# Kernel tuning notes

Hardware: AMD Instinct MI355X
Metric: run time of the kernel (lower is better)

## Reference

```python
import jax, jax.numpy as jnp
import numpy as np
from jax import lax

T, B, D = 1024, 32, 1024


def setup_inputs() -> dict:
    key = jax.random.key(0)
    k1, k2, k3, k4 = jax.random.split(key, 4)
    xav = (6.0 / (D + D)) ** 0.5  # xavier_uniform bound
    return {
        "x": jax.random.normal(k1, (T, B, D), dtype=jnp.float32),
        "h0": jnp.zeros((B, D), dtype=jnp.float32),
        "W_alpha": jax.random.uniform(k2, (D, D), minval=-xav, maxval=xav, dtype=jnp.float32),
        "d_alpha": jnp.full((D,), 0.1, dtype=jnp.float32),
        "b_alpha": jnp.full((D,), 2.0, dtype=jnp.float32),
        "W_x": jax.random.uniform(k3, (D, D), minval=-xav, maxval=xav, dtype=jnp.float32),
        "b_v": jnp.zeros((D,), dtype=jnp.float32),
    }


def reference(x, h0, W_alpha, d_alpha, b_alpha, W_x, b_v):
    # Precompute batched GEMMs once (x_t @ W.T), as in the original.
    alpha_x = jnp.einsum("tbd,ed->tbe", x, W_alpha)          # [T,B,D]
    v = jnp.tanh(jnp.einsum("tbd,ed->tbe", x, W_x) + b_v)    # [T,B,D]

    def step(h_prev, inp):
        ax_t, v_t = inp
        alpha = jax.nn.sigmoid(ax_t + d_alpha * h_prev + b_alpha)
        h_new = alpha * h_prev + (1.0 - alpha) * v_t
        out = h_new * h_new * jax.nn.sigmoid(h_new)  # h * silu(h)
        return h_new, (h_new, out)

    _, (hs, outs) = lax.scan(step, h0, (alpha_x, v))
    h = jnp.concatenate([h0[None], hs], axis=0)  # [T+1,B,D]
    return outs, h
```

## Files before the change

kernel.cpp:

```cpp
#include <hip/hip_runtime.h>
#include <hip/hip_bf16.h>
#include <stdint.h>

#define TT 1024
#define BB 32
#define DD 1024
#define MROWS (TT*BB)
#define NCOLS (2*DD)
#define KDIM  (DD)
#define SS (BB*DD)

typedef __attribute__((ext_vector_type(8))) short short8;
typedef __attribute__((ext_vector_type(4))) float f32x4;

__device__ __forceinline__ float bf2f(uint16_t u){
  union { uint32_t u; float f; } c; c.u = ((uint32_t)u) << 16; return c.f;
}
__device__ __forceinline__ uint16_t f2bf(float f){
  union { float f; uint32_t u; } c; c.f = f;
  uint32_t u = c.u;
  u += 0x7FFFu + ((u >> 16) & 1u);
  return (uint16_t)(u >> 16);
}
__device__ __forceinline__ float tanh_fast(float x){
  return 1.f - 2.f/(1.f + __expf(2.f*x));
}
__device__ __forceinline__ float sigmoid_fast(float x){
  return __builtin_amdgcn_rcpf(1.f + __expf(-x));
}

__global__ __launch_bounds__(256) void cvt_x_kernel(const float* __restrict__ x,
                                                    uint16_t* __restrict__ xb, int n4){
  int i = blockIdx.x * 256 + threadIdx.x;
  int stride = gridDim.x * 256;
  for (; i < n4; i += stride){
    float4 f = ((const float4*)x)[i];
    ushort4 o;
    o.x = f2bf(f.x); o.y = f2bf(f.y); o.z = f2bf(f.z); o.w = f2bf(f.w);
    ((ushort4*)xb)[i] = o;
  }
}

__global__ __launch_bounds__(256) void cvt_w_kernel(const float* __restrict__ Wa,
                                                    const float* __restrict__ Wx,
                                                    uint16_t* __restrict__ wc){
  int i = blockIdx.x * 256 + threadIdx.x;
  const int c    = i >> 8;
  const int col4 = i & 255;
  const int e = ((c >> 5) << 4) | (c & 15);
  const int s = (c >> 4) & 1;
  const float* src = (s ? Wx : Wa) + (size_t)e*DD + col4*4;
  float4 f = *(const float4*)src;
  ushort4 o;
  o.x = f2bf(f.x); o.y = f2bf(f.y); o.z = f2bf(f.z); o.w = f2bf(f.w);
  ((ushort4*)wc)[i] = o;
}

__global__ __launch_bounds__(512, 2) void gemm_dual(const uint16_t* __restrict__ xb,
                                                    const uint16_t* __restrict__ wc,
                                                    const float* __restrict__ bv,
                                                    uint32_t* __restrict__ av){
  __shared__ __align__(16) uint16_t lds[49152];
  char* ldsc = (char*)lds;

  const int tid  = threadIdx.x;
  const int lane = tid & 63;
  const int w    = tid >> 6;
  const int wm   = w >> 2;
  const int wn   = w & 3;
  const int fr   = lane & 15;
  const int fq   = lane >> 4;

  const int bid = blockIdx.x;
  const int bsw = (bid & 7) * 128 + (bid >> 3);
  const int bm  = (bsw >> 3) << 8;
  const int bn  = (bsw & 7) << 8;

  f32x4 acc[8][4] = {};

  const int srow = tid >> 2;
  const int soff = ((tid & 3) ^ ((tid >> 3) & 3)) * 8;

  #define STAGE_UNIT(kt, bufb, u) { \
    const uint16_t* s_ = ((u) < 2) ? xb : wc; \
    const int gb_ = ((u) < 2) ? bm : bn; \
    const int reg_ = ((u) < 2) ? 0 : 16384; \
    const int rb_ = ((u) & 1) * 128; \
    const uint16_t* g_ = s_ + (size_t)(gb_ + rb_ + srow)*KDIM + (kt)*32 + soff; \
    char* d_ = ldsc + (bufb) + reg_ + rb_*64 + w*1024; \
    __builtin_amdgcn_global_load_lds((const __attribute__((address_space(1))) void*)g_, \
                                     (__attribute__((address_space(3))) void*)d_, 16, 0, 0); \
  }

  const int slotoff = (fq ^ ((fr >> 1) & 3)) * 16;
  const int aoff0 = (wm*128 + fr)*64 + slotoff;
  const int boff0 = 16384 + (wn*64 + fr)*64 + slotoff;

  STAGE_UNIT(0, 0, 0) STAGE_UNIT(0, 0, 1) STAGE_UNIT(0, 0, 2) STAGE_UNIT(0, 0, 3)
  STAGE_UNIT(1, 32768, 0) STAGE_UNIT(1, 32768, 1) STAGE_UNIT(1, 32768, 2) STAGE_UNIT(1, 32768, 3)
  asm volatile("s_waitcnt vmcnt(4)" ::: "memory");
  __builtin_amdgcn_s_barrier();

  int bR = 0;
  for (int t = 0; t < 32; ++t){
    const int bRb = bR * 32768;
    const int bW  = (bR == 0) ? 2 : (bR - 1);
    const int bWb = bW * 32768;

    short8 aF[4], bF[4], aG[4];
    #pragma unroll
    for (int m = 0; m < 4; ++m)
      aF[m] = *(const short8*)(ldsc + bRb + aoff0 + m*1024);
    #pragma unroll
    for (int n = 0; n < 4; ++n)
      bF[n] = *(const short8*)(ldsc + bRb + boff0 + n*1024);
    if (t < 30){ STAGE_UNIT(t+2, bWb, 0) STAGE_UNIT(t+2, bWb, 1) }

    #pragma unroll
    for (int m = 0; m < 4; ++m)
      #pragma unroll
      for (int n = 0; n < 4; ++n)
        acc[m][n] = __builtin_amdgcn_mfma_f32_16x16x32_bf16(aF[m], bF[n], acc[m][n], 0, 0, 0);

    #pragma unroll
    for (int m = 0; m < 4; ++m)
      aG[m] = *(const short8*)(ldsc + bRb + aoff0 + 4096 + m*1024);
    if (t < 30){ STAGE_UNIT(t+2, bWb, 2) STAGE_UNIT(t+2, bWb, 3) }

    #pragma unroll
    for (int m = 0; m < 4; ++m)
      #pragma unroll
      for (int n = 0; n < 4; ++n)
        acc[4+m][n] = __builtin_amdgcn_mfma_f32_16x16x32_bf16(aG[m], bF[n], acc[4+m][n], 0, 0, 0);

    if (t < 30){
      asm volatile("s_waitcnt vmcnt(4)" ::: "memory");
      __builtin_amdgcn_s_barrier();
    } else if (t == 30){
      asm volatile("s_waitcnt vmcnt(0)" ::: "memory");
      __builtin_amdgcn_s_barrier();
    }

    bR = (bR == 2) ? 0 : (bR + 1);
  }
  #undef STAGE_UNIT

  const int ebase = (bn + wn*64) >> 1;
  const float bvn0 = bv[ebase + fr];
  const float bvn1 = bv[ebase + 16 + fr];
  #pragma unroll
  for (int m = 0; m < 8; ++m){
    #pragma unroll
    for (int j = 0; j < 4; ++j){
      const int row = bm + wm*128 + m*16 + fq*4 + j;
      const int tt = row >> 5, b = row & 31;
      const size_t base = (size_t)tt*SS + (size_t)b*DD;
      const float a0  = acc[m][0][j];
      const float vt0 = tanh_fast(acc[m][1][j] + bvn0);
      av[base + ebase + fr] = (uint32_t)f2bf(a0) | ((uint32_t)f2bf(vt0) << 16);
      const float a1  = acc[m][2][j];
      const float vt1 = tanh_fast(acc[m][3][j] + bvn1);
      av[base + ebase + 16 + fr] = (uint32_t)f2bf(a1) | ((uint32_t)f2bf(vt1) << 16);
    }
  }
}

#define SCAN_STEP(u, tcur)                                        \
  {                                                               \
    const float a_ = bf2f((uint16_t)(u));                         \
    const float v_ = bf2f((uint16_t)((u) >> 16));                 \
    const float al_ = sigmoid_fast(a_ + da*h + ba);               \
    h = al_*(h - v_) + v_;                                        \
    const float sg_ = sigmoid_fast(h);                            \
    __builtin_nontemporal_store(h*h*sg_, &outs[(size_t)(tcur)*SS + idx]); \
    __builtin_nontemporal_store(h, &houts[(size_t)((tcur)+1)*SS + idx]);  \
  }

__global__ __launch_bounds__(64) void scan_kernel(const uint32_t* __restrict__ av,
                                                  const float* __restrict__ h0,
                                                  const float* __restrict__ d_alpha,
                                                  const float* __restrict__ b_alpha,
                                                  float* __restrict__ outs,
                                                  float* __restrict__ houts){
  const int idx = blockIdx.x * 64 + threadIdx.x;
  const int e = idx & (DD-1);
  const float da = d_alpha[e];
  const float ba = b_alpha[e];
  float h = h0[idx];
  __builtin_nontemporal_store(h, &houts[idx]);

  uint32_t bufA[32], bufB[32];
  #pragma unroll
  for (int j = 0; j < 32; ++j) bufA[j] = av[(size_t)j*SS + idx];

  for (int t0 = 0; t0 < TT; t0 += 64){
    #pragma unroll
    for (int j = 0; j < 32; ++j) bufB[j] = av[(size_t)(t0+32+j)*SS + idx];
    #pragma unroll
    for (int j = 0; j < 32; ++j) SCAN_STEP(bufA[j], t0 + j);
    if (t0 + 64 < TT){
      #pragma unroll
      for (int j = 0; j < 32; ++j) bufA[j] = av[(size_t)(t0+64+j)*SS + idx];
    }
    #pragma unroll
    for (int j = 0; j < 32; ++j) SCAN_STEP(bufB[j], t0 + 32 + j);
  }
}

extern "C" void kernel_launch(void* const* d_in, const int* in_sizes, int n_in,
                              void* d_out, int out_size, void* d_ws, size_t ws_size,
                              hipStream_t stream){
  const float* x  = (const float*)d_in[0];
  const float* h0 = (const float*)d_in[1];
  const float* Wa = (const float*)d_in[2];
  const float* da = (const float*)d_in[3];
  const float* ba = (const float*)d_in[4];
  const float* Wx = (const float*)d_in[5];
  const float* bv = (const float*)d_in[6];

  float* outs  = (float*)d_out;
  float* houts = outs + (size_t)TT*BB*DD;

  uint8_t* ws = (uint8_t*)d_ws;
  uint16_t* wcb = (uint16_t*)ws;
  uint16_t* xb  = (uint16_t*)(ws + (size_t)NCOLS*KDIM*2);
  uint32_t* av  = (uint32_t*)(ws + (size_t)NCOLS*KDIM*2 + (size_t)MROWS*KDIM*2);

  hipLaunchKernelGGL(cvt_w_kernel, dim3(2048), dim3(256), 0, stream, Wa, Wx, wcb);
  hipLaunchKernelGGL(cvt_x_kernel, dim3(2048), dim3(256), 0, stream, x, xb, MROWS*KDIM/4);
  hipLaunchKernelGGL(gemm_dual, dim3((NCOLS/256)*(MROWS/256)), dim3(512), 0, stream,
                     xb, wcb, bv, av);
  hipLaunchKernelGGL(scan_kernel, dim3(SS/64), dim3(64), 0, stream,
                     av, h0, da, ba, outs, houts);
}
```

Measured before the change: 254.4 us.

## Use 4 waves with 128x128 warp tiles in dual GEMM

The GEMM block drops from 8 waves to 4. Each wave now computes a 128x128 output tile (8x8 MFMA fragments) instead of 128x64, which increases register-level reuse of the A and B fragments loaded from LDS. Each thread issues twice as many async global-to-LDS loads per stage, and the vmcnt waits are adjusted to match. The cost is much higher register pressure (256 accumulator floats per lane) and fewer waves available to hide latency, with occupancy bounded to one block per launch bound.

Measured after the change: 265.1 us. 4.2% more time.

```diff
diff --git a/kernel.cpp b/kernel.cpp
--- a/kernel.cpp
+++ b/kernel.cpp
@@ -56,7 +56,7 @@
   ((ushort4*)wc)[i] = o;
 }
 
-__global__ __launch_bounds__(512, 2) void gemm_dual(const uint16_t* __restrict__ xb,
+__global__ __launch_bounds__(256, 1) void gemm_dual(const uint16_t* __restrict__ xb,
                                                     const uint16_t* __restrict__ wc,
                                                     const float* __restrict__ bv,
                                                     uint32_t* __restrict__ av){
@@ -66,8 +66,8 @@
   const int tid  = threadIdx.x;
   const int lane = tid & 63;
   const int w    = tid >> 6;
-  const int wm   = w >> 2;
-  const int wn   = w & 3;
+  const int wm   = w >> 1;
+  const int wn   = w & 1;
   const int fr   = lane & 15;
   const int fq   = lane >> 4;
 
@@ -76,29 +76,30 @@
   const int bm  = (bsw >> 3) << 8;
   const int bn  = (bsw & 7) << 8;
 
-  f32x4 acc[8][4] = {};
-
-  const int srow = tid >> 2;
+  f32x4 acc[8][8] = {};
+
   const int soff = ((tid & 3) ^ ((tid >> 3) & 3)) * 8;
 
   #define STAGE_UNIT(kt, bufb, u) { \
-    const uint16_t* s_ = ((u) < 2) ? xb : wc; \
-    const int gb_ = ((u) < 2) ? bm : bn; \
-    const int reg_ = ((u) < 2) ? 0 : 16384; \
-    const int rb_ = ((u) & 1) * 128; \
-    const uint16_t* g_ = s_ + (size_t)(gb_ + rb_ + srow)*KDIM + (kt)*32 + soff; \
-    char* d_ = ldsc + (bufb) + reg_ + rb_*64 + w*1024; \
+    const uint16_t* s_ = ((u) < 4) ? xb : wc; \
+    const int gb_ = ((u) < 4) ? bm : bn; \
+    const int reg_ = ((u) < 4) ? 0 : 16384; \
+    const int rb_ = ((u) & 3) * 64; \
+    const uint16_t* g_ = s_ + (size_t)(gb_ + rb_ + (tid >> 2))*KDIM + (kt)*32 + soff; \
+    char* d_ = ldsc + (bufb) + reg_ + rb_*64 + tid*16; \
     __builtin_amdgcn_global_load_lds((const __attribute__((address_space(1))) void*)g_, \
                                      (__attribute__((address_space(3))) void*)d_, 16, 0, 0); \
   }
 
   const int slotoff = (fq ^ ((fr >> 1) & 3)) * 16;
   const int aoff0 = (wm*128 + fr)*64 + slotoff;
-  const int boff0 = 16384 + (wn*64 + fr)*64 + slotoff;
+  const int boff0 = 16384 + (wn*128 + fr)*64 + slotoff;
 
   STAGE_UNIT(0, 0, 0) STAGE_UNIT(0, 0, 1) STAGE_UNIT(0, 0, 2) STAGE_UNIT(0, 0, 3)
+  STAGE_UNIT(0, 0, 4) STAGE_UNIT(0, 0, 5) STAGE_UNIT(0, 0, 6) STAGE_UNIT(0, 0, 7)
   STAGE_UNIT(1, 32768, 0) STAGE_UNIT(1, 32768, 1) STAGE_UNIT(1, 32768, 2) STAGE_UNIT(1, 32768, 3)
-  asm volatile("s_waitcnt vmcnt(4)" ::: "memory");
+  STAGE_UNIT(1, 32768, 4) STAGE_UNIT(1, 32768, 5) STAGE_UNIT(1, 32768, 6) STAGE_UNIT(1, 32768, 7)
+  asm volatile("s_waitcnt vmcnt(8)" ::: "memory");
   __builtin_amdgcn_s_barrier();
 
   int bR = 0;
@@ -107,34 +108,26 @@
     const int bW  = (bR == 0) ? 2 : (bR - 1);
     const int bWb = bW * 32768;
 
-    short8 aF[4], bF[4], aG[4];
-    #pragma unroll
-    for (int m = 0; m < 4; ++m)
+    short8 aF[8], bF[8];
+    #pragma unroll
+    for (int m = 0; m < 8; ++m)
       aF[m] = *(const short8*)(ldsc + bRb + aoff0 + m*1024);
-    #pragma unroll
-    for (int n = 0; n < 4; ++n)
+    if (t < 30){ STAGE_UNIT(t+2, bWb, 0) STAGE_UNIT(t+2, bWb, 1)
+                 STAGE_UNIT(t+2, bWb, 2) STAGE_UNIT(t+2, bWb, 3) }
+    #pragma unroll
+    for (int n = 0; n < 8; ++n)
       bF[n] = *(const short8*)(ldsc + bRb + boff0 + n*1024);
-    if (t < 30){ STAGE_UNIT(t+2, bWb, 0) STAGE_UNIT(t+2, bWb, 1) }
-
-    #pragma unroll
-    for (int m = 0; m < 4; ++m)
+    if (t < 30){ STAGE_UNIT(t+2, bWb, 4) STAGE_UNIT(t+2, bWb, 5)
+                 STAGE_UNIT(t+2, bWb, 6) STAGE_UNIT(t+2, bWb, 7) }
+
+    #pragma unroll
+    for (int m = 0; m < 8; ++m)
       #pragma unroll
-      for (int n = 0; n < 4; ++n)
+      for (int n = 0; n < 8; ++n)
         acc[m][n] = __builtin_amdgcn_mfma_f32_16x16x32_bf16(aF[m], bF[n], acc[m][n], 0, 0, 0);
 
-    #pragma unroll
-    for (int m = 0; m < 4; ++m)
-      aG[m] = *(const short8*)(ldsc + bRb + aoff0 + 4096 + m*1024);
-    if (t < 30){ STAGE_UNIT(t+2, bWb, 2) STAGE_UNIT(t+2, bWb, 3) }
-
-    #pragma unroll
-    for (int m = 0; m < 4; ++m)
-      #pragma unroll
-      for (int n = 0; n < 4; ++n)
-        acc[4+m][n] = __builtin_amdgcn_mfma_f32_16x16x32_bf16(aG[m], bF[n], acc[4+m][n], 0, 0, 0);
-
     if (t < 30){
-      asm volatile("s_waitcnt vmcnt(4)" ::: "memory");
+      asm volatile("s_waitcnt vmcnt(8)" ::: "memory");
       __builtin_amdgcn_s_barrier();
     } else if (t == 30){
       asm volatile("s_waitcnt vmcnt(0)" ::: "memory");
@@ -145,9 +138,10 @@
   }
   #undef STAGE_UNIT
 
-  const int ebase = (bn + wn*64) >> 1;
-  const float bvn0 = bv[ebase + fr];
-  const float bvn1 = bv[ebase + 16 + fr];
+  const int ebase = (bn + wn*128) >> 1;
+  float bvn[4];
+  #pragma unroll
+  for (int p = 0; p < 4; ++p) bvn[p] = bv[ebase + p*16 + fr];
   #pragma unroll
   for (int m = 0; m < 8; ++m){
     #pragma unroll
@@ -155,12 +149,12 @@
       const int row = bm + wm*128 + m*16 + fq*4 + j;
       const int tt = row >> 5, b = row & 31;
       const size_t base = (size_t)tt*SS + (size_t)b*DD;
-      const float a0  = acc[m][0][j];
-      const float vt0 = tanh_fast(acc[m][1][j] + bvn0);
-      av[base + ebase + fr] = (uint32_t)f2bf(a0) | ((uint32_t)f2bf(vt0) << 16);
-      const float a1  = acc[m][2][j];
-      const float vt1 = tanh_fast(acc[m][3][j] + bvn1);
-      av[base + ebase + 16 + fr] = (uint32_t)f2bf(a1) | ((uint32_t)f2bf(vt1) << 16);
+      #pragma unroll
+      for (int p = 0; p < 4; ++p){
+        const float a  = acc[m][2*p][j];
+        const float vt = tanh_fast(acc[m][2*p+1][j] + bvn[p]);
+        av[base + ebase + p*16 + fr] = (uint32_t)f2bf(a) | ((uint32_t)f2bf(vt) << 16);
+      }
     }
   }
 }
@@ -228,7 +222,7 @@
 
   hipLaunchKernelGGL(cvt_w_kernel, dim3(2048), dim3(256), 0, stream, Wa, Wx, wcb);
   hipLaunchKernelGGL(cvt_x_kernel, dim3(2048), dim3(256), 0, stream, x, xb, MROWS*KDIM/4);
-  hipLaunchKernelGGL(gemm_dual, dim3((NCOLS/256)*(MROWS/256)), dim3(512), 0, stream,
+  hipLaunchKernelGGL(gemm_dual, dim3((NCOLS/256)*(MROWS/256)), dim3(256), 0, stream,
                      xb, wcb, bv, av);
   hipLaunchKernelGGL(scan_kernel, dim3(SS/64), dim3(64), 0, stream,
                      av, h0, da, ba, outs, houts);
```

## Fuse fp32-to-bf16 conversion of x into GEMM A-tile staging

Applied to the files above, without the earlier changes.

Removes the separate cvt_x kernel and its bf16 copy of x. The GEMM now loads fp32 x tiles into registers, converts them to bf16 in-kernel and writes them to LDS, while B tiles still use direct global-to-LDS loads. The pipeline wait counts and barriers are reworked to match. This saves a full read and write of the 128MB x tensor through the bf16 intermediate, at the cost of each GEMM block reading fp32 x (8 column blocks re-read it) and doing extra register and LDS-write work.

Result: no change. 259.5 us (+2.0%).

```diff
diff --git a/kernel.cpp b/kernel.cpp
--- a/kernel.cpp
+++ b/kernel.cpp
@@ -27,18 +27,6 @@
 }
 __device__ __forceinline__ float sigmoid_fast(float x){
   return __builtin_amdgcn_rcpf(1.f + __expf(-x));
-}
-
-__global__ __launch_bounds__(256) void cvt_x_kernel(const float* __restrict__ x,
-                                                    uint16_t* __restrict__ xb, int n4){
-  int i = blockIdx.x * 256 + threadIdx.x;
-  int stride = gridDim.x * 256;
-  for (; i < n4; i += stride){
-    float4 f = ((const float4*)x)[i];
-    ushort4 o;
-    o.x = f2bf(f.x); o.y = f2bf(f.y); o.z = f2bf(f.z); o.w = f2bf(f.w);
-    ((ushort4*)xb)[i] = o;
-  }
 }
 
 __global__ __launch_bounds__(256) void cvt_w_kernel(const float* __restrict__ Wa,
@@ -56,7 +44,7 @@
   ((ushort4*)wc)[i] = o;
 }
 
-__global__ __launch_bounds__(512, 2) void gemm_dual(const uint16_t* __restrict__ xb,
+__global__ __launch_bounds__(512, 2) void gemm_dual(const float* __restrict__ x,
                                                     const uint16_t* __restrict__ wc,
                                                     const float* __restrict__ bv,
                                                     uint32_t* __restrict__ av){
@@ -78,34 +66,62 @@
 
   f32x4 acc[8][4] = {};
 
-  const int srow = tid >> 2;
-  const int soff = ((tid & 3) ^ ((tid >> 3) & 3)) * 8;
-
-  #define STAGE_UNIT(kt, bufb, u) { \
-    const uint16_t* s_ = ((u) < 2) ? xb : wc; \
-    const int gb_ = ((u) < 2) ? bm : bn; \
-    const int reg_ = ((u) < 2) ? 0 : 16384; \
-    const int rb_ = ((u) & 1) * 128; \
-    const uint16_t* g_ = s_ + (size_t)(gb_ + rb_ + srow)*KDIM + (kt)*32 + soff; \
-    char* d_ = ldsc + (bufb) + reg_ + rb_*64 + w*1024; \
+  const int lslot = (tid & 3) ^ ((tid >> 3) & 3);
+
+  #define STAGE_B(kt, bufb, u) { \
+    const uint16_t* g_ = wc + (size_t)(bn + (u)*128 + (tid >> 2))*KDIM + (kt)*32 + lslot*8; \
+    char* d_ = ldsc + (bufb) + 16384 + (u)*8192 + w*1024; \
     __builtin_amdgcn_global_load_lds((const __attribute__((address_space(1))) void*)g_, \
                                      (__attribute__((address_space(3))) void*)d_, 16, 0, 0); \
   }
+
+  float4 a0lo, a0hi, a1lo, a1hi;
+  #define LOAD_A(kt) { \
+    const float* g0_ = x + (size_t)(bm + (tid >> 2))*KDIM + (kt)*32 + lslot*8; \
+    a0lo = *(const float4*)g0_; a0hi = *(const float4*)(g0_ + 4); \
+    const float* g1_ = g0_ + (size_t)128*KDIM; \
+    a1lo = *(const float4*)g1_; a1hi = *(const float4*)(g1_ + 4); \
+  }
+  #define WRITE_A(bufb) { \
+    union { short8 v; __hip_bfloat162 b[4]; } P0_, P1_; \
+    P0_.b[0] = __float22bfloat162_rn(make_float2(a0lo.x, a0lo.y)); \
+    P0_.b[1] = __float22bfloat162_rn(make_float2(a0lo.z, a0lo.w)); \
+    P0_.b[2] = __float22bfloat162_rn(make_float2(a0hi.x, a0hi.y)); \
+    P0_.b[3] = __float22bfloat162_rn(make_float2(a0hi.z, a0hi.w)); \
+    P1_.b[0] = __float22bfloat162_rn(make_float2(a1lo.x, a1lo.y)); \
+    P1_.b[1] = __float22bfloat162_rn(make_float2(a1lo.z, a1lo.w)); \
+    P1_.b[2] = __float22bfloat162_rn(make_float2(a1hi.x, a1hi.y)); \
+    P1_.b[3] = __float22bfloat162_rn(make_float2(a1hi.z, a1hi.w)); \
+    char* d0_ = ldsc + (bufb) + (tid >> 2)*64 + (tid & 3)*16; \
+    *(short8*)d0_ = P0_.v; \
+    *(short8*)(d0_ + 8192) = P1_.v; \
+  }
+  #define WALL asm volatile("" ::: "memory");
 
   const int slotoff = (fq ^ ((fr >> 1) & 3)) * 16;
   const int aoff0 = (wm*128 + fr)*64 + slotoff;
   const int boff0 = 16384 + (wn*64 + fr)*64 + slotoff;
 
-  STAGE_UNIT(0, 0, 0) STAGE_UNIT(0, 0, 1) STAGE_UNIT(0, 0, 2) STAGE_UNIT(0, 0, 3)
-  STAGE_UNIT(1, 32768, 0) STAGE_UNIT(1, 32768, 1) STAGE_UNIT(1, 32768, 2) STAGE_UNIT(1, 32768, 3)
-  asm volatile("s_waitcnt vmcnt(4)" ::: "memory");
+  LOAD_A(0) WALL
+  STAGE_B(0, 0, 0) STAGE_B(0, 0, 1) WALL
+  asm volatile("s_waitcnt vmcnt(2)" ::: "memory");
+  WRITE_A(0)
+  LOAD_A(1) WALL
+  STAGE_B(1, 32768, 0) STAGE_B(1, 32768, 1)
+  asm volatile("s_waitcnt vmcnt(6)" ::: "memory");
+  asm volatile("s_waitcnt lgkmcnt(0)" ::: "memory");
   __builtin_amdgcn_s_barrier();
 
   int bR = 0;
   for (int t = 0; t < 32; ++t){
-    const int bRb = bR * 32768;
-    const int bW  = (bR == 0) ? 2 : (bR - 1);
-    const int bWb = bW * 32768;
+    const int bRb  = bR * 32768;
+    const int bW1b = ((bR == 2) ? 0 : bR + 1) * 32768;
+    const int bW2b = ((bR == 0) ? 2 : bR - 1) * 32768;
+
+    if (t < 31){
+      asm volatile("s_waitcnt vmcnt(2)" ::: "memory");
+      WRITE_A(bW1b)
+    }
 
     short8 aF[4], bF[4], aG[4];
     #pragma unroll
@@ -114,7 +130,7 @@
     #pragma unroll
     for (int n = 0; n < 4; ++n)
       bF[n] = *(const short8*)(ldsc + bRb + boff0 + n*1024);
-    if (t < 30){ STAGE_UNIT(t+2, bWb, 0) STAGE_UNIT(t+2, bWb, 1) }
+    if (t < 30){ LOAD_A(t+2) WALL STAGE_B(t+2, bW2b, 0) STAGE_B(t+2, bW2b, 1) }
 
     #pragma unroll
     for (int m = 0; m < 4; ++m)
@@ -125,7 +141,6 @@
     #pragma unroll
     for (int m = 0; m < 4; ++m)
       aG[m] = *(const short8*)(ldsc + bRb + aoff0 + 4096 + m*1024);
-    if (t < 30){ STAGE_UNIT(t+2, bWb, 2) STAGE_UNIT(t+2, bWb, 3) }
 
     #pragma unroll
     for (int m = 0; m < 4; ++m)
@@ -134,16 +149,21 @@
         acc[4+m][n] = __builtin_amdgcn_mfma_f32_16x16x32_bf16(aG[m], bF[n], acc[4+m][n], 0, 0, 0);
 
     if (t < 30){
-      asm volatile("s_waitcnt vmcnt(4)" ::: "memory");
-      __builtin_amdgcn_s_barrier();
+      asm volatile("s_waitcnt vmcnt(6)" ::: "memory");
     } else if (t == 30){
       asm volatile("s_waitcnt vmcnt(0)" ::: "memory");
+    }
+    if (t < 31){
+      asm volatile("s_waitcnt lgkmcnt(0)" ::: "memory");
       __builtin_amdgcn_s_barrier();
     }
 
-    bR = (bR == 2) ? 0 : (bR + 1);
-  }
-  #undef STAGE_UNIT
+    bR = (bR == 2) ? 0 : bR + 1;
+  }
+  #undef STAGE_B
+  #undef LOAD_A
+  #undef WRITE_A
+  #undef WALL
 
   const int ebase = (bn + wn*64) >> 1;
   const float bvn0 = bv[ebase + fr];
@@ -223,13 +243,11 @@
 
   uint8_t* ws = (uint8_t*)d_ws;
   uint16_t* wcb = (uint16_t*)ws;
-  uint16_t* xb  = (uint16_t*)(ws + (size_t)NCOLS*KDIM*2);
-  uint32_t* av  = (uint32_t*)(ws + (size_t)NCOLS*KDIM*2 + (size_t)MROWS*KDIM*2);
+  uint32_t* av  = (uint32_t*)(ws + (size_t)NCOLS*KDIM*2);
 
   hipLaunchKernelGGL(cvt_w_kernel, dim3(2048), dim3(256), 0, stream, Wa, Wx, wcb);
-  hipLaunchKernelGGL(cvt_x_kernel, dim3(2048), dim3(256), 0, stream, x, xb, MROWS*KDIM/4);
   hipLaunchKernelGGL(gemm_dual, dim3((NCOLS/256)*(MROWS/256)), dim3(512), 0, stream,
-                     xb, wcb, bv, av);
+                     x, wcb, bv, av);
   hipLaunchKernelGGL(scan_kernel, dim3(SS/64), dim3(64), 0, stream,
                      av, h0, da, ba, outs, houts);
 }
```
